# Optimization experiments

Hardware: AMD Instinct MI355X
Metric: run time of the kernel (lower is better)

The kernel has to match this reference:

```python
import jax, jax.numpy as jnp
import numpy as np
import math

HEAD_SIZE = 64

def setup_inputs() -> dict:
    key = jax.random.key(0)
    k0, k1, k2, k3 = jax.random.split(key, 4)
    B, T, E, H = 4, 4096, 1024, HEAD_SIZE
    return {
        "x": jax.random.normal(k0, (B, T, E), dtype=jnp.float32),
        "Wq": jax.random.normal(k1, (E, H), dtype=jnp.float32) * (1.0 / math.sqrt(E)),
        "Wk": jax.random.normal(k2, (E, H), dtype=jnp.float32) * (1.0 / math.sqrt(E)),
        "Wv": jax.random.normal(k3, (E, H), dtype=jnp.float32) * (1.0 / math.sqrt(E)),
    }

def reference(x, Wq, Wk, Wv):
    # Single-head attention; faithful to source: softmax FIRST, then divide by sqrt(head_size)
    T = x.shape[-2]
    q = x @ Wq  # [B,T,H]
    k = x @ Wk
    v = x @ Wv
    scores = jnp.einsum('bth,bsh->bts', q, k)  # [B,T,T]
    # 'encoder' mask in this repo = lower-triangular (causal)
    causal = jnp.tril(jnp.ones((T, T), dtype=bool))
    scores = jnp.where(causal, scores, -jnp.inf)
    attn = jax.nn.softmax(scores, axis=-1) / jnp.sqrt(jnp.float32(q.shape[-1]))
    return jnp.einsum('bts,bsh->bth', attn, v)
```

## Files before the change

kernel.cpp:

```cpp
#include <hip/hip_runtime.h>
#include <math.h>

#define BB 4
#define TT 4096
#define EE 1024
#define HH 64

typedef __attribute__((ext_vector_type(8))) short bf16x8;
typedef _Float16 f16x8 __attribute__((ext_vector_type(8)));
typedef __attribute__((ext_vector_type(4))) float f32x4;

#define MFMA16(a, b, c)  __builtin_amdgcn_mfma_f32_16x16x32_bf16(a, b, c, 0, 0, 0)
#define MFMA16F(a, b, c) __builtin_amdgcn_mfma_f32_16x16x32_f16(a, b, c, 0, 0, 0)

__device__ __forceinline__ unsigned short f2bf_rne(float f) {
    unsigned u = __float_as_uint(f);
    unsigned r = u + 0x7fffu + ((u >> 16) & 1u);
    return (unsigned short)(r >> 16);
}
__device__ __forceinline__ float bf2f(unsigned short h) {
    return __uint_as_float(((unsigned)h) << 16);
}
__device__ __forceinline__ unsigned short f2h(float f) {
    union { _Float16 h; unsigned short u; } cv;
    cv.h = (_Float16)f;
    return cv.u;
}

__device__ __forceinline__ void async_copy16(const void* g, void* l) {
    __builtin_amdgcn_global_load_lds(
        (const __attribute__((address_space(1))) void*)g,
        (__attribute__((address_space(3))) void*)l, 16, 0, 0);
}
template<int N>
__device__ __forceinline__ void wait_vm() {
    __builtin_amdgcn_s_waitcnt(0x0f70 | (N & 15) | ((N >> 4) << 14));
}

__global__ __launch_bounds__(256) void wprep_kernel(
    const float* __restrict__ Wq, const float* __restrict__ Wk,
    const float* __restrict__ Wv,
    unsigned short* __restrict__ wt_hi, unsigned short* __restrict__ wt_lo)
{
    __shared__ float ts[64][65];
    const int which = blockIdx.x >> 4;
    const int e0 = (blockIdx.x & 15) * 64;
    const float* W = (which == 0) ? Wq : ((which == 1) ? Wk : Wv);
    const int t = threadIdx.x;
    const int h = t & 63;
    #pragma unroll
    for (int p = 0; p < 16; p++) {
        const int er = (t >> 6) + p * 4;
        ts[er][h] = W[(size_t)(e0 + er) * 64 + h];
    }
    __syncthreads();
    const int ew = t & 63;
    #pragma unroll
    for (int p = 0; p < 16; p++) {
        const int hh = (t >> 6) + p * 4;
        const float f = ts[ew][hh];
        const unsigned short hb = f2bf_rne(f);
        const unsigned short lb = f2bf_rne(f - bf2f(hb));
        const size_t o = (size_t)(which * 64 + hh) * 1024 + e0 + ew;
        wt_hi[o] = hb;
        wt_lo[o] = lb;
    }
}

__global__ __launch_bounds__(512) void proj_kernel(
    const float* __restrict__ x,
    const unsigned short* __restrict__ wt_hi, const unsigned short* __restrict__ wt_lo,
    unsigned short* __restrict__ qhf, unsigned short* __restrict__ qlf,
    unsigned short* __restrict__ kf, unsigned short* __restrict__ vt)
{
    __shared__ __align__(16) unsigned char smem[147456];
    const int tid = threadIdx.x;
    const int w = tid >> 6, lane = tid & 63;
    const int quad = lane >> 4, li = lane & 15;
    const int tg = w & 3, eh = w >> 2;
    const int row0 = (int)blockIdx.x * 64;
    const int tok = row0 + tg * 16 + li;
    const int s0 = ((int)blockIdx.x >> 3) & 15;

    f32x4 acc[12];
    #pragma unroll
    for (int mt = 0; mt < 12; mt++) acc[mt] = (f32x4){0.f, 0.f, 0.f, 0.f};

    const float* xr = x + (size_t)tok * EE + eh * 512 + quad * 8;

    const int r_l = lane >> 3, sl = lane & 7;
    const int cg = sl ^ r_l;
    const unsigned short* mat = (cg < 4) ? wt_hi : wt_lo;
    const int ce = (cg & 3) * 8;
    const int sA = (quad ^ (li & 7)) * 8;
    const int sB = ((4 + quad) ^ (li & 7)) * 8;

    auto dma_step = [&](int e0, unsigned char* dstbase) {
        #pragma unroll
        for (int ii = 0; ii < 6; ii++) {
            const int i = w * 6 + ii;
            const int ehc = i / 24;
            const int within = i % 24;
            const int row = within * 8 + r_l;
            const unsigned short* src = mat + (size_t)row * EE + ehc * 512 + e0 + ce;
            async_copy16(src, dstbase + ehc * 24576 + within * 1024);
        }
    };

    const int eo0 = ((s0 + 0) & 15) * 32;
    const int eo1 = ((s0 + 1) & 15) * 32;

    dma_step(eo0, smem);
    float4 fc0 = *(const float4*)(xr + eo0);
    float4 fc1 = *(const float4*)(xr + eo0 + 4);
    dma_step(eo1, smem + 49152);
    float4 fn0 = *(const float4*)(xr + eo1);
    float4 fn1 = *(const float4*)(xr + eo1 + 4);
    float4 ff0, ff1;

    for (int s = 0; s < 16; s++) {
        if (s + 2 < 16) {
            const int eo2 = ((s0 + s + 2) & 15) * 32;
            dma_step(eo2, smem + ((s + 2) % 3) * 49152);
            ff0 = *(const float4*)(xr + eo2);
            ff1 = *(const float4*)(xr + eo2 + 4);
            wait_vm<16>();
        } else if (s + 1 < 16) {
            wait_vm<8>();
        } else {
            wait_vm<0>();
        }
        __builtin_amdgcn_s_barrier();

        float fv[8] = {fc0.x, fc0.y, fc0.z, fc0.w, fc1.x, fc1.y, fc1.z, fc1.w};
        bf16x8 bh, bl;
        #pragma unroll
        for (int jj = 0; jj < 8; jj++) {
            unsigned short hb = f2bf_rne(fv[jj]);
            bh[jj] = (short)hb;
            bl[jj] = (short)f2bf_rne(fv[jj] - bf2f(hb));
        }
        const unsigned short* Wbase =
            (const unsigned short*)(smem + (s % 3) * 49152 + eh * 24576);
        #pragma unroll
        for (int mt = 0; mt < 12; mt++) {
            const unsigned short* rb = Wbase + (mt * 16 + li) * 64;
            bf16x8 Ah = *(const bf16x8*)(rb + sA);
            bf16x8 Al = *(const bf16x8*)(rb + sB);
            acc[mt] = MFMA16(Ah, bh, acc[mt]);
            acc[mt] = MFMA16(Ah, bl, acc[mt]);
            acc[mt] = MFMA16(Al, bh, acc[mt]);
        }
        __builtin_amdgcn_s_barrier();
        fc0 = fn0; fc1 = fn1; fn0 = ff0; fn1 = ff1;
    }

    float* Red = (float*)smem;
    if (eh == 1) {
        #pragma unroll
        for (int mt = 0; mt < 12; mt++)
            #pragma unroll
            for (int r = 0; r < 4; r++)
                Red[(size_t)(tg * 192 + mt * 16 + quad * 4 + r) * 17 + li] = acc[mt][r];
    }
    __syncthreads();
    if (eh == 0) {
        #pragma unroll
        for (int mt = 0; mt < 12; mt++)
            #pragma unroll
            for (int r = 0; r < 4; r++)
                acc[mt][r] += Red[(size_t)(tg * 192 + mt * 16 + quad * 4 + r) * 17 + li];
        const int bb = tok >> 12, tloc = tok & 4095;
        #pragma unroll
        for (int mt = 0; mt < 12; mt++) {
            if (mt < 4) {
                const int h = (mt & 3) * 16 + quad * 4;
                ushort4 hi4, lo4; float f; _Float16 hh;
                union { _Float16 h; unsigned short u; } cv;
                f = acc[mt][0]; hh = (_Float16)f; cv.h = hh; hi4.x = cv.u; lo4.x = f2h(f - (float)hh);
                f = acc[mt][1]; hh = (_Float16)f; cv.h = hh; hi4.y = cv.u; lo4.y = f2h(f - (float)hh);
                f = acc[mt][2]; hh = (_Float16)f; cv.h = hh; hi4.z = cv.u; lo4.z = f2h(f - (float)hh);
                f = acc[mt][3]; hh = (_Float16)f; cv.h = hh; hi4.w = cv.u; lo4.w = f2h(f - (float)hh);
                const size_t o = (size_t)tok * 64 + h;
                *(ushort4*)(qhf + o) = hi4;
                *(ushort4*)(qlf + o) = lo4;
            } else if (mt < 8) {
                const int h = (mt & 3) * 16 + quad * 4;
                ushort4 k4;
                k4.x = f2h(acc[mt][0]); k4.y = f2h(acc[mt][1]);
                k4.z = f2h(acc[mt][2]); k4.w = f2h(acc[mt][3]);
                *(ushort4*)(kf + (size_t)tok * 64 + h) = k4;
            } else {
                const int hv = (mt - 8) * 16 + quad * 4;
                #pragma unroll
                for (int r = 0; r < 4; r++)
                    vt[((size_t)(bb * 64 + hv + r) << 12) + tloc] = f2bf_rne(acc[mt][r]);
            }
        }
    }
}

__global__ __launch_bounds__(512) void flash_kernel(
    const unsigned short* __restrict__ qhf, const unsigned short* __restrict__ qlf,
    const unsigned short* __restrict__ kf,
    const unsigned short* __restrict__ vt, float* __restrict__ out)
{
    __shared__ __align__(16) unsigned char smem[119808];
    const int tid = threadIdx.x;
    const int w = tid >> 6, lane = tid & 63;
    const int quad = lane >> 4, li = lane & 15;
    const int lb = (int)blockIdx.x;
    const int b  = (lb & 7) >> 1;
    const int bx = ((lb >> 3) << 1) | (lb & 1);
    const float SM = 20.0f;

    const _Float16* kb = (const _Float16*)kf + ((size_t)b << 18);
    const unsigned short* vtb = vt + ((size_t)b << 18) + (size_t)li * 4096 + quad * 8;

    unsigned char* kbase = smem + w * 12288;
    unsigned short* PsA = (unsigned short*)(smem + 98304 + w * 2560);
    unsigned short* PsB = PsA + 640;
    float* Op = (float*)smem;
    float* Ml = (float*)(smem + 118784);

    const int r_l8 = lane >> 3, s8 = lane & 7;
    const int slf0 = ((quad)     ^ (li & 7)) * 8;
    const int slf1 = ((4 + quad) ^ (li & 7)) * 8;

    auto dma_tile = [&](int k0, unsigned char* dst) {
        #pragma unroll
        for (int i = 0; i < 4; i++) {
            const int row = i * 8 + r_l8;
            const int c = s8 ^ r_l8;
            async_copy16(kb + (size_t)(k0 + row) * 64 + c * 8, dst + i * 1024);
        }
    };

    #pragma unroll 1
    for (int phase = 0; phase < 2; phase++) {
        const int g = phase ? (127 - bx) : bx;
        const int q0 = g * 32;
        const int n_kt = g + 1;
        const int tok0 = q0 + li, tok1 = tok0 + 16;

        const size_t qo0 = ((size_t)(b << 12) + tok0) * 64 + quad * 8;
        const size_t qo1 = qo0 + 16 * 64;
        const _Float16* qh_p = (const _Float16*)qhf;
        const _Float16* ql_p = (const _Float16*)qlf;
        const f16x8 QhA0 = *(const f16x8*)(qh_p + qo0);
        const f16x8 QhA1 = *(const f16x8*)(qh_p + qo0 + 32);
        const f16x8 QlA0 = *(const f16x8*)(ql_p + qo0);
        const f16x8 QlA1 = *(const f16x8*)(ql_p + qo0 + 32);
        const f16x8 QhB0 = *(const f16x8*)(qh_p + qo1);
        const f16x8 QhB1 = *(const f16x8*)(qh_p + qo1 + 32);
        const f16x8 QlB0 = *(const f16x8*)(ql_p + qo1);
        const f16x8 QlB1 = *(const f16x8*)(ql_p + qo1 + 32);

        f32x4 accA[4], accB[4];
        #pragma unroll
        for (int mt = 0; mt < 4; mt++) {
            accA[mt] = (f32x4){0.f, 0.f, 0.f, 0.f};
            accB[mt] = (f32x4){0.f, 0.f, 0.f, 0.f};
        }
        float lA = 0.f, lB = 0.f;

        bf16x8 Vc[4], Vn[4], Vm[4];
        if (w < n_kt) {
            dma_tile(w * 32, kbase);
            #pragma unroll
            for (int hf = 0; hf < 4; hf++)
                Vc[hf] = *(const bf16x8*)(vtb + (size_t)hf * 65536 + w * 32);
        }
        if (w + 8 < n_kt) {
            dma_tile((w + 8) * 32, kbase + 4096);
            #pragma unroll
            for (int hf = 0; hf < 4; hf++)
                Vn[hf] = *(const bf16x8*)(vtb + (size_t)hf * 65536 + (w + 8) * 32);
        }

        int n_it = 0;
        for (int kt = w; kt < n_kt; kt += 8, n_it++) {
            const int k0 = kt * 32;
            const int slot = n_it % 3;

            if (kt + 16 < n_kt) {
                const int s2p = slot + 2;
                const int slot2 = (s2p >= 3) ? s2p - 3 : s2p;
                dma_tile((kt + 16) * 32, kbase + slot2 * 4096);
                #pragma unroll
                for (int hf = 0; hf < 4; hf++)
                    Vm[hf] = *(const bf16x8*)(vtb + (size_t)hf * 65536 + (kt + 16) * 32);
                wait_vm<16>();
            } else if (kt + 8 < n_kt) {
                wait_vm<8>();
            } else {
                wait_vm<0>();
            }
            const _Float16* Kw = (const _Float16*)(kbase + slot * 4096);

            f32x4 sA[2], sB[2];
            #pragma unroll
            for (int jf = 0; jf < 2; jf++) {
                const _Float16* rb = Kw + (jf * 16 + li) * 64;
                f16x8 K0 = *(const f16x8*)(rb + slf0);
                f16x8 K1 = *(const f16x8*)(rb + slf1);
                f32x4 a = (f32x4){0.f, 0.f, 0.f, 0.f};
                a = MFMA16F(K0, QhA0, a);
                a = MFMA16F(K1, QhA1, a);
                a = MFMA16F(K0, QlA0, a);
                a = MFMA16F(K1, QlA1, a);
                sA[jf] = a;
                f32x4 c2 = (f32x4){0.f, 0.f, 0.f, 0.f};
                c2 = MFMA16F(K0, QhB0, c2);
                c2 = MFMA16F(K1, QhB1, c2);
                c2 = MFMA16F(K0, QlB0, c2);
                c2 = MFMA16F(K1, QlB1, c2);
                sB[jf] = c2;
            }

            if (kt == n_kt - 1) {
                #pragma unroll
                for (int jf = 0; jf < 2; jf++)
                    #pragma unroll
                    for (int r = 0; r < 4; r++) {
                        const int j = k0 + jf * 16 + quad * 4 + r;
                        if (j > tok0) sA[jf][r] = -1e30f;
                        if (j > tok1) sB[jf][r] = -1e30f;
                    }
            }

            #pragma unroll
            for (int jf = 0; jf < 2; jf++)
                #pragma unroll
                for (int r = 0; r < 4; r++) {
                    sA[jf][r] = __expf(sA[jf][r] - SM); lA += sA[jf][r];
                    sB[jf][r] = __expf(sB[jf][r] - SM); lB += sB[jf][r];
                }

            #pragma unroll
            for (int jf = 0; jf < 2; jf++) {
                ushort4 pa, pb;
                pa.x = f2bf_rne(sA[jf][0]); pa.y = f2bf_rne(sA[jf][1]);
                pa.z = f2bf_rne(sA[jf][2]); pa.w = f2bf_rne(sA[jf][3]);
                pb.x = f2bf_rne(sB[jf][0]); pb.y = f2bf_rne(sB[jf][1]);
                pb.z = f2bf_rne(sB[jf][2]); pb.w = f2bf_rne(sB[jf][3]);
                *(ushort4*)&PsA[li * 40 + jf * 16 + quad * 4] = pa;
                *(ushort4*)&PsB[li * 40 + jf * 16 + quad * 4] = pb;
            }
            const bf16x8 PA = *(const bf16x8*)&PsA[li * 40 + quad * 8];
            const bf16x8 PB = *(const bf16x8*)&PsB[li * 40 + quad * 8];

            #pragma unroll
            for (int hf = 0; hf < 4; hf++) {
                accA[hf] = MFMA16(Vc[hf], PA, accA[hf]);
                accB[hf] = MFMA16(Vc[hf], PB, accB[hf]);
            }
            #pragma unroll
            for (int hf = 0; hf < 4; hf++) { Vc[hf] = Vn[hf]; Vn[hf] = Vm[hf]; }
        }

        lA += __shfl_xor(lA, 16); lA += __shfl_xor(lA, 32);
        lB += __shfl_xor(lB, 16); lB += __shfl_xor(lB, 32);

        __syncthreads();
        #pragma unroll
        for (int mt = 0; mt < 4; mt++)
            #pragma unroll
            for (int r = 0; r < 4; r++) {
                Op[(size_t)w * 2112 + (mt * 16 + quad * 4 + r) * 33 + li]      = accA[mt][r];
                Op[(size_t)w * 2112 + (mt * 16 + quad * 4 + r) * 33 + li + 16] = accB[mt][r];
            }
        if (quad == 0) {
            Ml[w * 32 + li]      = lA;
            Ml[w * 32 + 16 + li] = lB;
        }
        __syncthreads();

        const int i  = tid >> 4;
        const int hc = (tid & 15) * 4;
        float l = 0.f;
        #pragma unroll
        for (int ww = 0; ww < 8; ww++) l += Ml[ww * 32 + i];
        const float inv = 1.0f / (l * 8.0f);
        float4 o = {0.f, 0.f, 0.f, 0.f};
        #pragma unroll
        for (int ww = 0; ww < 8; ww++) {
            const float* base = Op + (size_t)ww * 2112;
            o.x += base[(hc + 0) * 33 + i];
            o.y += base[(hc + 1) * 33 + i];
            o.z += base[(hc + 2) * 33 + i];
            o.w += base[(hc + 3) * 33 + i];
        }
        o.x *= inv; o.y *= inv; o.z *= inv; o.w *= inv;
        *(float4*)(out + ((size_t)(b << 12) + q0 + i) * 64 + hc) = o;
        __syncthreads();
    }
}

extern "C" void kernel_launch(void* const* d_in, const int* in_sizes, int n_in,
                              void* d_out, int out_size, void* d_ws, size_t ws_size,
                              hipStream_t stream)
{
    const float* x  = (const float*)d_in[0];
    const float* Wq = (const float*)d_in[1];
    const float* Wk = (const float*)d_in[2];
    const float* Wv = (const float*)d_in[3];
    float* out = (float*)d_out;

    const size_t n_tok = (size_t)BB * TT * HH;
    unsigned short* qhf = (unsigned short*)d_ws;
    unsigned short* qlf = qhf + n_tok;
    unsigned short* kf  = qlf + n_tok;
    unsigned short* vt  = kf + n_tok;
    unsigned short* wt_hi = vt + n_tok;
    unsigned short* wt_lo = wt_hi + 192 * 1024;

    wprep_kernel<<<48, 256, 0, stream>>>(Wq, Wk, Wv, wt_hi, wt_lo);
    proj_kernel<<<(BB * TT) / 64, 512, 0, stream>>>(x, wt_hi, wt_lo,
                                                    qhf, qlf, kf, vt);
    flash_kernel<<<256, 512, 0, stream>>>(qhf, qlf, kf, vt, out);
}
```

Before: 157.9 us.

## Use single fp16 weights with split fp16 activations in projection

```diff
diff --git a/kernel.cpp b/kernel.cpp
--- a/kernel.cpp
+++ b/kernel.cpp
@@ -40,7 +40,7 @@
 __global__ __launch_bounds__(256) void wprep_kernel(
     const float* __restrict__ Wq, const float* __restrict__ Wk,
     const float* __restrict__ Wv,
-    unsigned short* __restrict__ wt_hi, unsigned short* __restrict__ wt_lo)
+    unsigned short* __restrict__ wt)
 {
     __shared__ float ts[64][65];
     const int which = blockIdx.x >> 4;
@@ -59,17 +59,14 @@
     for (int p = 0; p < 16; p++) {
         const int hh = (t >> 6) + p * 4;
         const float f = ts[ew][hh];
-        const unsigned short hb = f2bf_rne(f);
-        const unsigned short lb = f2bf_rne(f - bf2f(hb));
         const size_t o = (size_t)(which * 64 + hh) * 1024 + e0 + ew;
-        wt_hi[o] = hb;
-        wt_lo[o] = lb;
+        wt[o] = f2h(f);
     }
 }
 
 __global__ __launch_bounds__(512) void proj_kernel(
     const float* __restrict__ x,
-    const unsigned short* __restrict__ wt_hi, const unsigned short* __restrict__ wt_lo,
+    const unsigned short* __restrict__ wt,
     unsigned short* __restrict__ qhf, unsigned short* __restrict__ qlf,
     unsigned short* __restrict__ kf, unsigned short* __restrict__ vt)
 {
@@ -80,7 +77,6 @@
     const int tg = w & 3, eh = w >> 2;
     const int row0 = (int)blockIdx.x * 64;
     const int tok = row0 + tg * 16 + li;
-    const int s0 = ((int)blockIdx.x >> 3) & 15;
 
     f32x4 acc[12];
     #pragma unroll
@@ -89,11 +85,7 @@
     const float* xr = x + (size_t)tok * EE + eh * 512 + quad * 8;
 
     const int r_l = lane >> 3, sl = lane & 7;
-    const int cg = sl ^ r_l;
-    const unsigned short* mat = (cg < 4) ? wt_hi : wt_lo;
-    const int ce = (cg & 3) * 8;
-    const int sA = (quad ^ (li & 7)) * 8;
-    const int sB = ((4 + quad) ^ (li & 7)) * 8;
+    const int c_l = sl ^ r_l;
 
     auto dma_step = [&](int e0, unsigned char* dstbase) {
         #pragma unroll
@@ -102,57 +94,69 @@
             const int ehc = i / 24;
             const int within = i % 24;
             const int row = within * 8 + r_l;
-            const unsigned short* src = mat + (size_t)row * EE + ehc * 512 + e0 + ce;
+            const unsigned short* src = wt + (size_t)row * EE + ehc * 512 + e0 + c_l * 8;
             async_copy16(src, dstbase + ehc * 24576 + within * 1024);
         }
     };
 
-    const int eo0 = ((s0 + 0) & 15) * 32;
-    const int eo1 = ((s0 + 1) & 15) * 32;
-
-    dma_step(eo0, smem);
-    float4 fc0 = *(const float4*)(xr + eo0);
-    float4 fc1 = *(const float4*)(xr + eo0 + 4);
-    dma_step(eo1, smem + 49152);
-    float4 fn0 = *(const float4*)(xr + eo1);
-    float4 fn1 = *(const float4*)(xr + eo1 + 4);
-    float4 ff0, ff1;
-
-    for (int s = 0; s < 16; s++) {
-        if (s + 2 < 16) {
-            const int eo2 = ((s0 + s + 2) & 15) * 32;
-            dma_step(eo2, smem + ((s + 2) % 3) * 49152);
-            ff0 = *(const float4*)(xr + eo2);
-            ff1 = *(const float4*)(xr + eo2 + 4);
-            wait_vm<16>();
-        } else if (s + 1 < 16) {
-            wait_vm<8>();
+    const int r7 = li & 7;
+    const int slot0 = ((0 + quad) ^ r7) * 8;
+    const int slot1 = ((4 + quad) ^ r7) * 8;
+
+    dma_step(0, smem);
+    float4 fc0 = *(const float4*)(xr + 0);
+    float4 fc1 = *(const float4*)(xr + 4);
+    float4 fc2 = *(const float4*)(xr + 32);
+    float4 fc3 = *(const float4*)(xr + 36);
+    dma_step(64, smem + 49152);
+    float4 fn0 = *(const float4*)(xr + 64);
+    float4 fn1 = *(const float4*)(xr + 68);
+    float4 fn2 = *(const float4*)(xr + 96);
+    float4 fn3 = *(const float4*)(xr + 100);
+    float4 ff0, ff1, ff2, ff3;
+
+    for (int s = 0; s < 8; s++) {
+        if (s + 2 < 8) {
+            const int e2 = (s + 2) * 64;
+            dma_step(e2, smem + ((s + 2) % 3) * 49152);
+            ff0 = *(const float4*)(xr + e2);
+            ff1 = *(const float4*)(xr + e2 + 4);
+            ff2 = *(const float4*)(xr + e2 + 32);
+            ff3 = *(const float4*)(xr + e2 + 36);
+            wait_vm<20>();
+        } else if (s + 1 < 8) {
+            wait_vm<10>();
         } else {
             wait_vm<0>();
         }
         __builtin_amdgcn_s_barrier();
 
-        float fv[8] = {fc0.x, fc0.y, fc0.z, fc0.w, fc1.x, fc1.y, fc1.z, fc1.w};
-        bf16x8 bh, bl;
-        #pragma unroll
-        for (int jj = 0; jj < 8; jj++) {
-            unsigned short hb = f2bf_rne(fv[jj]);
-            bh[jj] = (short)hb;
-            bl[jj] = (short)f2bf_rne(fv[jj] - bf2f(hb));
-        }
-        const unsigned short* Wbase =
-            (const unsigned short*)(smem + (s % 3) * 49152 + eh * 24576);
-        #pragma unroll
-        for (int mt = 0; mt < 12; mt++) {
-            const unsigned short* rb = Wbase + (mt * 16 + li) * 64;
-            bf16x8 Ah = *(const bf16x8*)(rb + sA);
-            bf16x8 Al = *(const bf16x8*)(rb + sB);
-            acc[mt] = MFMA16(Ah, bh, acc[mt]);
-            acc[mt] = MFMA16(Ah, bl, acc[mt]);
-            acc[mt] = MFMA16(Al, bh, acc[mt]);
+        const _Float16* Wbase = (const _Float16*)(smem + (s % 3) * 49152)
+                                + eh * 12288 + (li >> 3) * 512 + r7 * 64;
+
+        #pragma unroll
+        for (int ks = 0; ks < 2; ks++) {
+            const float4 va = ks ? fc2 : fc0;
+            const float4 vb = ks ? fc3 : fc1;
+            float fv[8] = {va.x, va.y, va.z, va.w, vb.x, vb.y, vb.z, vb.w};
+            f16x8 bh, bl;
+            #pragma unroll
+            for (int jj = 0; jj < 8; jj++) {
+                const _Float16 hh = (_Float16)fv[jj];
+                bh[jj] = hh;
+                bl[jj] = (_Float16)(fv[jj] - (float)hh);
+            }
+            const int slot = ks ? slot1 : slot0;
+            #pragma unroll
+            for (int mt = 0; mt < 12; mt++) {
+                const f16x8 A = *(const f16x8*)(Wbase + mt * 1024 + slot);
+                acc[mt] = MFMA16F(A, bh, acc[mt]);
+                acc[mt] = MFMA16F(A, bl, acc[mt]);
+            }
         }
         __builtin_amdgcn_s_barrier();
-        fc0 = fn0; fc1 = fn1; fn0 = ff0; fn1 = ff1;
+        fc0 = fn0; fc1 = fn1; fc2 = fn2; fc3 = fn3;
+        fn0 = ff0; fn1 = ff1; fn2 = ff2; fn3 = ff3;
     }
 
     float* Red = (float*)smem;
@@ -412,11 +416,10 @@
     unsigned short* qlf = qhf + n_tok;
     unsigned short* kf  = qlf + n_tok;
     unsigned short* vt  = kf + n_tok;
-    unsigned short* wt_hi = vt + n_tok;
-    unsigned short* wt_lo = wt_hi + 192 * 1024;
-
-    wprep_kernel<<<48, 256, 0, stream>>>(Wq, Wk, Wv, wt_hi, wt_lo);
-    proj_kernel<<<(BB * TT) / 64, 512, 0, stream>>>(x, wt_hi, wt_lo,
+    unsigned short* wt  = vt + n_tok;
+
+    wprep_kernel<<<48, 256, 0, stream>>>(Wq, Wk, Wv, wt);
+    proj_kernel<<<(BB * TT) / 64, 512, 0, stream>>>(x, wt,
                                                     qhf, qlf, kf, vt);
     flash_kernel<<<256, 512, 0, stream>>>(qhf, qlf, kf, vt, out);
 }
```

Result: faster. 146.5 us (median of 2 runs) (-7.2%).
